# Kernel tuning notes

Hardware: AMD Instinct MI355X
Metric: run time of the kernel (lower is better)

The kernel has to match this reference:

```python
import jax, jax.numpy as jnp
import numpy as np

B, S_SRC, D, H, DH, FF, L, V, W, NG = 2, 4093, 768, 12, 64, 3072, 2, 50265, 256, 3
S = S_SRC + NG            # 4096, multiple of one-sided window W=256
NC = S // W               # 16 chunks
EPS = 1e-5
CLS_IDS = (50261, 50262, 50263)
NEG = -1e9


def setup_inputs() -> dict:
    key = jax.random.key(0)
    ks = jax.random.split(key, 16)
    std = 0.02
    inp = {
        "src": jax.random.randint(ks[0], (B, S_SRC), 0, 50260),
        "mask_src": jnp.ones((B, S_SRC), dtype=bool),
        "cluster_sizes": jax.random.randint(ks[1], (B,), 0, 16),
        "word_emb": jax.random.normal(ks[2], (V, D), jnp.float32) * std,
        "pos_emb": jax.random.normal(ks[3], (S, D), jnp.float32) * std,
        "emb_ln": jnp.stack([jnp.ones((D,)), jnp.zeros((D,))]),              # [2,D] scale,bias
        "attn_w": jax.random.normal(ks[4], (L, 7, D, D), jnp.float32) * std,  # q,k,v,qg,kg,vg,o
        "attn_b": jnp.zeros((L, 7, D), jnp.float32),
        "ln_p": jnp.stack([jnp.stack([jnp.ones((D,)), jnp.zeros((D,)), jnp.ones((D,)), jnp.zeros((D,))]) for _ in range(L)]),  # [L,4,D]
        "ffn_w1": jax.random.normal(ks[5], (L, D, FF), jnp.float32) * std,
        "ffn_b1": jnp.zeros((L, FF), jnp.float32),
        "ffn_w2": jax.random.normal(ks[6], (L, FF, D), jnp.float32) * std,
        "ffn_b2": jnp.zeros((L, D), jnp.float32),
        "cls_w": jax.random.normal(ks[7], (3, D), jnp.float32) * std,
        "cls_b": jnp.zeros((3,), jnp.float32),
    }
    return inp


def _ln(x, scale, bias):
    mu = jnp.mean(x, axis=-1, keepdims=True)
    var = jnp.mean(jnp.square(x - mu), axis=-1, keepdims=True)
    return (x - mu) * jax.lax.rsqrt(var + EPS) * scale + bias


def _encoder(ids, mask, word_emb, pos_emb, emb_ln, attn_w, attn_b, ln_p,
             ffn_w1, ffn_b1, ffn_w2, ffn_b2):
    x = _ln(word_emb[ids] + pos_emb[None, :S], emb_ln[0], emb_ln[1])  # [B,S,D]

    # static banded-attention index structure (chunk of W queries sees 3W keys)
    idx = np.arange(NC)[:, None] * W + np.arange(3 * W)[None, :]  # into padded seq
    kp = idx - W                                                   # absolute key pos
    valid = (kp >= 0) & (kp < S)
    kpc = jnp.asarray(np.clip(kp, 0, S - 1))
    qpos = np.arange(W)[:, None]
    band = jnp.asarray(np.abs(np.arange(3 * W)[None, :] - W - qpos) <= W)  # [W,3W]
    # global & padding keys removed from windowed attention (HF semantics)
    keymask = mask[:, kpc] & jnp.asarray(valid)[None] & jnp.asarray(kp >= NG)[None]  # [B,NC,3W]
    allowed = band[None, None] & keymask[:, :, None, :]  # [B,NC,W,3W]
    scale = 1.0 / np.sqrt(DH)

    def layer(x, p):
        aw, ab, lnp, w1, b1, w2, b2 = p
        def proj(i):
            return (x @ aw[i] + ab[i]).reshape(B, S, H, DH).transpose(0, 2, 1, 3)
        q = proj(0) * scale
        k = proj(1)
        v = proj(2)
        kpad = jnp.pad(k, ((0, 0), (0, 0), (W, W), (0, 0)))
        vpad = jnp.pad(v, ((0, 0), (0, 0), (W, W), (0, 0)))
        Kc = kpad[:, :, kpc + W]  # [B,H,NC,3W,DH] (kpc+W indexes padded)
        Vc = vpad[:, :, kpc + W]
        qc = q.reshape(B, H, NC, W, DH)
        s_loc = jnp.einsum('bhcqd,bhckd->bhcqk', qc, Kc)
        s_loc = jnp.where(allowed[:, None], s_loc, NEG)
        s_glb = jnp.einsum('bhcqd,bhgd->bhcqg', qc, k[:, :, :NG])  # all tokens -> global keys
        probs = jax.nn.softmax(jnp.concatenate([s_glb, s_loc], axis=-1), axis=-1)
        out = (jnp.einsum('bhcqg,bhgd->bhcqd', probs[..., :NG], v[:, :, :NG])
               + jnp.einsum('bhcqk,bhckd->bhcqd', probs[..., NG:], Vc))
        out = out.reshape(B, H, S, DH)
        # global query rows: full attention with global q/k/v projections
        qg = ((x[:, :NG] @ aw[3] + ab[3]).reshape(B, NG, H, DH)) * scale
        kg = (x @ aw[4] + ab[4]).reshape(B, S, H, DH)
        vg = (x @ aw[5] + ab[5]).reshape(B, S, H, DH)
        sg = jnp.einsum('bghd,bshd->bhgs', qg, kg)
        sg = jnp.where(mask[:, None, None, :], sg, NEG)
        og = jnp.einsum('bhgs,bshd->bhgd', jax.nn.softmax(sg, axis=-1), vg)
        out = out.at[:, :, :NG, :].set(og)
        out = out.transpose(0, 2, 1, 3).reshape(B, S, D)
        xa = _ln(x + out @ aw[6] + ab[6], lnp[0], lnp[1])
        h = jax.nn.gelu(xa @ w1 + b1, approximate=False)
        return _ln(xa + h @ w2 + b2, lnp[2], lnp[3]), None

    x, _ = jax.lax.scan(layer, x, (attn_w, attn_b, ln_p, ffn_w1, ffn_b1, ffn_w2, ffn_b2))
    return x


def reference(src, mask_src, cluster_sizes, word_emb, pos_emb, emb_ln, attn_w,
              attn_b, ln_p, ffn_w1, ffn_b1, ffn_w2, ffn_b2, cls_w, cls_b):
    ids = jnp.concatenate([jnp.broadcast_to(jnp.asarray(CLS_IDS), (B, NG)), src], axis=1)
    mask = jnp.concatenate([jnp.ones((B, NG), dtype=bool), mask_src], axis=1)
    h = _encoder(ids, mask, word_emb, pos_emb, emb_ln, attn_w, attn_b, ln_p,
                 ffn_w1, ffn_b1, ffn_w2, ffn_b2)  # [B,S,D]
    mf = mask.astype(h.dtype)
    scores = [jax.nn.sigmoid(h[:, i] @ cls_w[i] + cls_b[i]) * mf[:, i] for i in range(3)]
    verd, pros, cons = (s[:, None] for s in scores)
    return verd, pros, cons, mf[:, 0][:, None]
```

## Files before the change

### kernel.cpp

```cpp
#include <hip/hip_runtime.h>
#include <hip/hip_bf16.h>
#include <math.h>

#define B_    2
#define SSRC_ 4093
#define D_    768
#define H_    12
#define DH_   64
#define FF_   3072
#define NG_   3
#define W_    256
#define S_    4096
#define NC_   16
#define NSPLIT_ 16
#define QB_   128

typedef __attribute__((ext_vector_type(8))) short frag_ab;
typedef __attribute__((ext_vector_type(4))) float f32x4;

#define GL16(gp, lp) __builtin_amdgcn_global_load_lds( \
    (const __attribute__((address_space(1))) void*)(gp), \
    (__attribute__((address_space(3))) void*)(lp), 16, 0, 0)

__device__ __forceinline__ float bflo(unsigned int w) {
    union { float f; unsigned int i; } c; c.i = w << 16; return c.f;
}
__device__ __forceinline__ float bfhi(unsigned int w) {
    union { float f; unsigned int i; } c; c.i = w & 0xffff0000u; return c.f;
}
__device__ __forceinline__ void unp8(uint4 t, float* o) {
    o[0] = bflo(t.x); o[1] = bfhi(t.x); o[2] = bflo(t.y); o[3] = bfhi(t.y);
    o[4] = bflo(t.z); o[5] = bfhi(t.z); o[6] = bflo(t.w); o[7] = bfhi(t.w);
}
__device__ __forceinline__ unsigned short f2bfu(float x) {
    __hip_bfloat16 h = __float2bfloat16(x);
    return *reinterpret_cast<unsigned short*>(&h);
}

__device__ __forceinline__ float block_sum(float v, float* red) {
    int tid = threadIdx.x;
    red[tid] = v;
    __syncthreads();
#pragma unroll
    for (int off = 128; off >= 1; off >>= 1) {
        if (tid < off) red[tid] += red[tid + off];
        __syncthreads();
    }
    float r = red[0];
    __syncthreads();
    return r;
}

__device__ __forceinline__ float block_max(float v, float* red) {
    int tid = threadIdx.x;
    red[tid] = v;
    __syncthreads();
#pragma unroll
    for (int off = 128; off >= 1; off >>= 1) {
        if (tid < off) red[tid] = fmaxf(red[tid], red[tid + off]);
        __syncthreads();
    }
    float r = red[0];
    __syncthreads();
    return r;
}

__device__ __forceinline__ void storeO(float* p, float v) { *p = v; }
__device__ __forceinline__ void storeO(__hip_bfloat16* p, float v) { *p = __float2bfloat16(v); }

__global__ __launch_bounds__(256) void embed_ln_k(
    const int* __restrict__ src, const float* __restrict__ we,
    const float* __restrict__ pe, const float* __restrict__ gam,
    const float* __restrict__ bet, float* __restrict__ X,
    __hip_bfloat16* __restrict__ Xb) {
    __shared__ float red[256];
    int row = blockIdx.x;
    int b = row >> 12;
    int s = row & (S_ - 1);
    int tid = threadIdx.x;
    int id = (s < NG_) ? (50261 + s) : src[b * SSRC_ + (s - NG_)];
    const float* wr = we + (size_t)id * D_;
    const float* pr = pe + (size_t)s * D_;
    float v[3];
    float lsum = 0.f;
#pragma unroll
    for (int j = 0; j < 3; ++j) {
        int c = tid + j * 256;
        v[j] = wr[c] + pr[c];
        lsum += v[j];
    }
    float mu = block_sum(lsum, red) * (1.0f / 768.0f);
    float ls2 = 0.f;
#pragma unroll
    for (int j = 0; j < 3; ++j) { float d = v[j] - mu; ls2 += d * d; }
    float var = block_sum(ls2, red) * (1.0f / 768.0f);
    float rs = rsqrtf(var + 1e-5f);
    float* xr = X + (size_t)row * D_;
    __hip_bfloat16* xbr = Xb + (size_t)row * D_;
#pragma unroll
    for (int j = 0; j < 3; ++j) {
        int c = tid + j * 256;
        float o = (v[j] - mu) * rs * gam[c] + bet[c];
        xr[c] = o;
        xbr[c] = __float2bfloat16(o);
    }
}

__global__ __launch_bounds__(256) void residual_ln_k(
    const float* __restrict__ x, const float* __restrict__ y,
    const float* __restrict__ y2, const float* __restrict__ gam,
    const float* __restrict__ bet, float* __restrict__ out,
    __hip_bfloat16* __restrict__ outb) {
    __shared__ float red[256];
    int row = blockIdx.x;
    int tid = threadIdx.x;
    const float* xr = x + (size_t)row * D_;
    const float* yr = y + (size_t)row * D_;
    const float* y2r = y2 ? y2 + (size_t)row * D_ : nullptr;
    float v[3];
    float lsum = 0.f;
#pragma unroll
    for (int j = 0; j < 3; ++j) {
        int c = tid + j * 256;
        v[j] = xr[c] + yr[c];
        if (y2r) v[j] += y2r[c];
        lsum += v[j];
    }
    float mu = block_sum(lsum, red) * (1.0f / 768.0f);
    float ls2 = 0.f;
#pragma unroll
    for (int j = 0; j < 3; ++j) { float d = v[j] - mu; ls2 += d * d; }
    float var = block_sum(ls2, red) * (1.0f / 768.0f);
    float rs = rsqrtf(var + 1e-5f);
    float* orow = out + (size_t)row * D_;
    __hip_bfloat16* obr = outb ? outb + (size_t)row * D_ : nullptr;
#pragma unroll
    for (int j = 0; j < 3; ++j) {
        int c = tid + j * 256;
        float o = (v[j] - mu) * rs * gam[c] + bet[c];
        orow[c] = o;
        if (obr) obr[c] = __float2bfloat16(o);
    }
}

__global__ __launch_bounds__(256) void convt_k(
    const float* __restrict__ W, __hip_bfloat16* __restrict__ WT,
    int K, int N, int npb ) {
    __shared__ float tile[32][33];
    int mat = blockIdx.x / npb;
    int bx = blockIdx.x - mat * npb;
    int by = blockIdx.y;
    const float* Wm = W + (size_t)mat * K * N;
    __hip_bfloat16* WTm = WT + (size_t)mat * N * K;
    int tx = threadIdx.x & 31, ty = threadIdx.x >> 5;
#pragma unroll
    for (int i = 0; i < 32; i += 8)
        tile[ty + i][tx] = Wm[(size_t)(by * 32 + ty + i) * N + bx * 32 + tx];
    __syncthreads();
#pragma unroll
    for (int i = 0; i < 32; i += 8)
        WTm[(size_t)(bx * 32 + ty + i) * K + by * 32 + tx] = __float2bfloat16(tile[tx][ty + i]);
}

__global__ void pack_bias_k(const float* __restrict__ ab, float* __restrict__ dst) {
    int j = blockIdx.x * 256 + threadIdx.x;
    if (j >= 5 * 768) return;
    int mat = j / 768, c = j - mat * 768;
    int i = (mat < 3) ? mat : mat + 1;
    dst[j] = ab[i * 768 + c];
}

template <int EPI, int SPLIT>
__global__ __launch_bounds__(256) void mfma_gemm_k(
    const __hip_bfloat16* __restrict__ A, const __hip_bfloat16* __restrict__ BT,
    const float* __restrict__ bias, void* __restrict__ Cout,
    int M, int N, int K, size_t matstride) {
    __shared__ __align__(16) __hip_bfloat16 As[4096];
    __shared__ __align__(16) __hip_bfloat16 Bs[4096];
    int tid = threadIdx.x;
    int lane = tid & 63;
    int w = tid >> 6, wr = w >> 1, wc = w & 1;
    int brow = blockIdx.y * 128, bcol = blockIdx.x * 128;
    int z = blockIdx.z, nz = gridDim.z;
    int Kz = K / nz;
    int r0 = tid >> 2;
    int k0 = (((tid & 3) ^ (r0 & 3)) * 8);
    const __hip_bfloat16* Ag0 = A + (size_t)(brow + r0) * K + z * Kz + k0;
    const __hip_bfloat16* Ag1 = Ag0 + (size_t)64 * K;
    const __hip_bfloat16* Bg0 = BT + (size_t)(bcol + r0) * K + z * Kz + k0;
    const __hip_bfloat16* Bg1 = Bg0 + (size_t)64 * K;
    __hip_bfloat16* lA0 = &As[tid * 8];
    __hip_bfloat16* lA1 = &As[tid * 8 + 2048];
    __hip_bfloat16* lB0 = &Bs[tid * 8];
    __hip_bfloat16* lB1 = &Bs[tid * 8 + 2048];

    f32x4 acc[4][4];
#pragma unroll
    for (int m = 0; m < 4; ++m)
#pragma unroll
        for (int n = 0; n < 4; ++n) acc[m][n] = (f32x4){0.f, 0.f, 0.f, 0.f};

    int l15 = lane & 15, kb = lane >> 4;
    int xkb = kb ^ (l15 & 3);
    int aoff = (wr * 64 + l15) * 32 + xkb * 8;
    int boff = (wc * 64 + l15) * 32 + xkb * 8;

    for (int kt = 0; kt < Kz; kt += 32) {
        GL16(Ag0 + kt, lA0);
        GL16(Ag1 + kt, lA1);
        GL16(Bg0 + kt, lB0);
        GL16(Bg1 + kt, lB1);
        __syncthreads();
        frag_ab af[4], bf[4];
#pragma unroll
        for (int m = 0; m < 4; ++m) af[m] = *(const frag_ab*)&As[aoff + m * 512];
#pragma unroll
        for (int n = 0; n < 4; ++n) bf[n] = *(const frag_ab*)&Bs[boff + n * 512];
        __builtin_amdgcn_s_setprio(1);
#pragma unroll
        for (int m = 0; m < 4; ++m)
#pragma unroll
            for (int n = 0; n < 4; ++n)
                acc[m][n] = __builtin_amdgcn_mfma_f32_16x16x32_bf16(af[m], bf[n], acc[m][n], 0, 0, 0);
        __builtin_amdgcn_s_setprio(0);
        __syncthreads();
    }

    size_t zoff = (size_t)z * M * N;
#pragma unroll
    for (int m = 0; m < 4; ++m) {
        int rowb = brow + wr * 64 + m * 16 + (lane >> 4) * 4;
#pragma unroll
        for (int n = 0; n < 4; ++n) {
            int col = bcol + wc * 64 + n * 16 + l15;
            float bv = (z == 0) ? bias[col] : 0.f;
#pragma unroll
            for (int r = 0; r < 4; ++r) {
                float v = acc[m][n][r] + bv;
                size_t idx;
                if (SPLIT) {
                    int mat = col / 768;
                    idx = (size_t)mat * matstride + (size_t)(rowb + r) * 768 + (col - mat * 768);
                } else {
                    idx = zoff + (size_t)(rowb + r) * N + col;
                }
                if (EPI == 0) {
                    ((float*)Cout)[idx] = v;
                } else if (EPI == 1) {
                    ((__hip_bfloat16*)Cout)[idx] = __float2bfloat16(v);
                } else {
                    float g = 0.5f * v * (1.0f + erff(v * 0.70710678118654752f));
                    ((__hip_bfloat16*)Cout)[idx] = __float2bfloat16(g);
                }
            }
        }
    }
}

__global__ __launch_bounds__(256) void skinny_gemm_k(
    const float* __restrict__ A, const float* __restrict__ W,
    float* __restrict__ partial, int N, int K) {
    __shared__ float Asl[6][64];
    __shared__ float red[4][6][64];
    int tid = threadIdx.x;
    int cl = tid & 63;
    int kg = tid >> 6;
    int col = blockIdx.x * 64 + cl;
    int k0 = blockIdx.y * 64;
    for (int i = tid; i < 6 * 64; i += 256)
        Asl[i >> 6][i & 63] = A[(size_t)(i >> 6) * K + k0 + (i & 63)];
    __syncthreads();
    float acc[6] = {0.f, 0.f, 0.f, 0.f, 0.f, 0.f};
#pragma unroll
    for (int kk = 0; kk < 16; ++kk) {
        int k = kg * 16 + kk;
        float wv = W[(size_t)(k0 + k) * N + col];
#pragma unroll
        for (int m = 0; m < 6; ++m) acc[m] += Asl[m][k] * wv;
    }
#pragma unroll
    for (int m = 0; m < 6; ++m) red[kg][m][cl] = acc[m];
    __syncthreads();
    for (int i = tid; i < 6 * 64; i += 256) {
        int m = i >> 6, lane = i & 63;
        float s = red[0][m][lane] + red[1][m][lane] + red[2][m][lane] + red[3][m][lane];
        partial[(size_t)blockIdx.y * 6 * N + (size_t)m * N + blockIdx.x * 64 + lane] = s;
    }
}

__global__ __launch_bounds__(256) void skinny_reduce_k(
    const float* __restrict__ partial, const float* __restrict__ bias,
    float* __restrict__ outp, int N, int KS, int gelu) {
    int idx = blockIdx.x * 256 + threadIdx.x;
    if (idx >= 6 * N) return;
    int m = idx / N, col = idx - m * N;
    float s = bias[col];
    for (int kb = 0; kb < KS; ++kb)
        s += partial[(size_t)kb * 6 * N + (size_t)m * N + col];
    if (gelu) s = 0.5f * s * (1.0f + erff(s * 0.70710678118654752f));
    outp[(size_t)m * N + col] = s;
}

__global__ __launch_bounds__(256, 1) void local_attn_k(
    const __hip_bfloat16* __restrict__ Q, const __hip_bfloat16* __restrict__ K,
    const __hip_bfloat16* __restrict__ V, __hip_bfloat16* __restrict__ O) {
    __shared__ __align__(16) __hip_bfloat16 K_lds[64 * 72];
    __shared__ __align__(16) __hip_bfloat16 VT_lds[64 * 72];
    __shared__ __align__(16) __hip_bfloat16 P_lds[4][16 * 72];

    const int cq = blockIdx.x, h = blockIdx.y, b = blockIdx.z;
    const int tid = threadIdx.x;
    const int lane = tid & 63;
    const int w = tid >> 6;
    const int l15 = lane & 15, g4 = lane >> 4;
    const int cbase = cq * QB_;

    frag_ab qf[2][2];
#pragma unroll
    for (int qt = 0; qt < 2; ++qt) {
        int qa = cbase + w * 32 + qt * 16 + l15;
        const __hip_bfloat16* qp = Q + (size_t)(b * S_ + qa) * D_ + h * DH_ + g4 * 8;
        qf[qt][0] = *(const frag_ab*)qp;
        qf[qt][1] = *(const frag_ab*)(qp + 32);
    }

    f32x4 o[2][4];
#pragma unroll
    for (int qt = 0; qt < 2; ++qt)
#pragma unroll
        for (int dt = 0; dt < 4; ++dt) o[qt][dt] = (f32x4){0.f, 0.f, 0.f, 0.f};
    float mrun[2] = {-1e30f, -1e30f};
    float lrun[2] = {0.f, 0.f};

    int kw0 = cbase - W_; if (kw0 < 0) kw0 = 0;
    int kw1 = cbase + QB_ + W_; if (kw1 > S_) kw1 = S_;
    int ntiles = (kw1 - kw0) >> 6;

    char* Pw = (char*)P_lds[w];

    for (int t = 0; t < ntiles; ++t) {
        int k0 = kw0 + t * 64;
        __syncthreads();
        {
            const __hip_bfloat16* Kg = K + (size_t)(b * S_ + k0) * D_ + h * DH_;
            const __hip_bfloat16* Vg = V + (size_t)(b * S_ + k0) * D_ + h * DH_;
#pragma unroll
            for (int it = 0; it < 2; ++it) {
                int idx = tid + it * 256;
                int kk = idx >> 3, d0 = (idx & 7) * 8;
                uint4 kv = *(const uint4*)(Kg + (size_t)kk * D_ + d0);
                *(uint4*)&K_lds[kk * 72 + d0] = kv;
                uint4 vv = *(const uint4*)(Vg + (size_t)kk * D_ + d0);
                unsigned short vs[8];
                *(uint4*)vs = vv;
#pragma unroll
                for (int j = 0; j < 8; ++j) {
                    int dd = d0 + j;
                    int boff = dd * 144 + ((kk * 2) ^ (((dd >> 3) & 7) << 4));
                    *(unsigned short*)((char*)VT_lds + boff) = vs[j];
                }
            }
        }
        __syncthreads();

        frag_ab kf[4][2];
#pragma unroll
        for (int kt = 0; kt < 4; ++kt) {
            const char* kp = (const char*)K_lds + (kt * 16 + l15) * 144 + g4 * 16;
            kf[kt][0] = *(const frag_ab*)kp;
            kf[kt][1] = *(const frag_ab*)(kp + 64);
        }
        frag_ab vf[4][2];
#pragma unroll
        for (int dt = 0; dt < 4; ++dt) {
            int drow = dt * 16 + l15;
            int swz = ((drow >> 3) & 7) << 4;
            const char* vp = (const char*)VT_lds + drow * 144;
            vf[dt][0] = *(const frag_ab*)(vp + ((g4 * 16) ^ swz));
            vf[dt][1] = *(const frag_ab*)(vp + ((g4 * 16 + 64) ^ swz));
        }

#pragma unroll
        for (int qt = 0; qt < 2; ++qt) {
            f32x4 st[4];
            __builtin_amdgcn_s_setprio(1);
#pragma unroll
            for (int kt = 0; kt < 4; ++kt) {
                f32x4 z = (f32x4){0.f, 0.f, 0.f, 0.f};
                z = __builtin_amdgcn_mfma_f32_16x16x32_bf16(kf[kt][0], qf[qt][0], z, 0, 0, 0);
                z = __builtin_amdgcn_mfma_f32_16x16x32_bf16(kf[kt][1], qf[qt][1], z, 0, 0, 0);
                st[kt] = z;
            }
            __builtin_amdgcn_s_setprio(0);
            int qa = cbase + w * 32 + qt * 16 + l15;
            float sv[16];
            float mx = -1e30f;
#pragma unroll
            for (int kt = 0; kt < 4; ++kt)
#pragma unroll
                for (int r = 0; r < 4; ++r) {
                    int ka = k0 + kt * 16 + g4 * 4 + r;
                    float s = st[kt][r] * 0.125f;
                    bool bad = (ka < NG_) | (ka - qa > W_) | (qa - ka > W_);
                    s = bad ? -1e30f : s;
                    sv[kt * 4 + r] = s;
                    mx = fmaxf(mx, s);
                }
            mx = fmaxf(mx, __shfl_xor(mx, 16));
            mx = fmaxf(mx, __shfl_xor(mx, 32));
            float mnew = fmaxf(fmaxf(mrun[qt], mx), -60.0f);
            if (__any(mnew != mrun[qt])) {
                float fsc = __expf(mrun[qt] - mnew);
                mrun[qt] = mnew;
#pragma unroll
                for (int dt = 0; dt < 4; ++dt) o[qt][dt] *= fsc;
                lrun[qt] *= fsc;
            }
            float psum = 0.f;
            unsigned short pb[16];
#pragma unroll
            for (int i = 0; i < 16; ++i) {
                float p = __expf(sv[i] - mrun[qt]);
                psum += p;
                pb[i] = f2bfu(p);
            }
            psum += __shfl_xor(psum, 16);
            psum += __shfl_xor(psum, 32);
            lrun[qt] += psum;
#pragma unroll
            for (int kt = 0; kt < 4; ++kt)
#pragma unroll
                for (int rp = 0; rp < 2; ++rp) {
                    unsigned vpk = (unsigned)pb[kt * 4 + rp * 2] | ((unsigned)pb[kt * 4 + rp * 2 + 1] << 16);
                    int kloc = kt * 16 + g4 * 4 + rp * 2;
                    *(unsigned*)(Pw + l15 * 144 + kloc * 2) = vpk;
                }
            frag_ab pf0 = *(const frag_ab*)(Pw + l15 * 144 + g4 * 16);
            frag_ab pf1 = *(const frag_ab*)(Pw + l15 * 144 + g4 * 16 + 64);
            __builtin_amdgcn_s_setprio(1);
#pragma unroll
            for (int dt = 0; dt < 4; ++dt) {
                o[qt][dt] = __builtin_amdgcn_mfma_f32_16x16x32_bf16(vf[dt][0], pf0, o[qt][dt], 0, 0, 0);
                o[qt][dt] = __builtin_amdgcn_mfma_f32_16x16x32_bf16(vf[dt][1], pf1, o[qt][dt], 0, 0, 0);
            }
            __builtin_amdgcn_s_setprio(0);
        }
    }

    uint4 kgc[3][2];
    uint2 vgd[3][4];
#pragma unroll
    for (int gk = 0; gk < NG_; ++gk) {
        const __hip_bfloat16* kp = K + (size_t)(b * S_ + gk) * D_ + h * DH_ + g4 * 8;
        kgc[gk][0] = *(const uint4*)kp;
        kgc[gk][1] = *(const uint4*)(kp + 32);
        const __hip_bfloat16* vp = V + (size_t)(b * S_ + gk) * D_ + h * DH_ + g4 * 4;
#pragma unroll
        for (int dt = 0; dt < 4; ++dt)
            vgd[gk][dt] = *(const uint2*)(vp + dt * 16);
    }
#pragma unroll
    for (int qt = 0; qt < 2; ++qt) {
        float sg[3];
#pragma unroll
        for (int gk = 0; gk < NG_; ++gk) {
            float part = 0.f;
#pragma unroll
            for (int s = 0; s < 2; ++s) {
                uint4 qw = *(uint4*)&qf[qt][s];
                uint4 kw = kgc[gk][s];
                part += bflo(qw.x) * bflo(kw.x) + bfhi(qw.x) * bfhi(kw.x);
                part += bflo(qw.y) * bflo(kw.y) + bfhi(qw.y) * bfhi(kw.y);
                part += bflo(qw.z) * bflo(kw.z) + bfhi(qw.z) * bfhi(kw.z);
                part += bflo(qw.w) * bflo(kw.w) + bfhi(qw.w) * bfhi(kw.w);
            }
            part += __shfl_xor(part, 16);
            part += __shfl_xor(part, 32);
            sg[gk] = part * 0.125f;
        }
        float mx3 = fmaxf(fmaxf(sg[0], sg[1]), sg[2]);
        float mnew = fmaxf(fmaxf(mrun[qt], mx3), -60.0f);
        float fsc = __expf(mrun[qt] - mnew);
        mrun[qt] = mnew;
#pragma unroll
        for (int dt = 0; dt < 4; ++dt) o[qt][dt] *= fsc;
        lrun[qt] *= fsc;
        float pg[3];
        float psum = 0.f;
#pragma unroll
        for (int gk = 0; gk < NG_; ++gk) { pg[gk] = __expf(sg[gk] - mnew); psum += pg[gk]; }
        lrun[qt] += psum;
#pragma unroll
        for (int dt = 0; dt < 4; ++dt) {
#pragma unroll
            for (int gk = 0; gk < NG_; ++gk) {
                uint2 vv = vgd[gk][dt];
                o[qt][dt][0] += pg[gk] * bflo(vv.x);
                o[qt][dt][1] += pg[gk] * bfhi(vv.x);
                o[qt][dt][2] += pg[gk] * bflo(vv.y);
                o[qt][dt][3] += pg[gk] * bfhi(vv.y);
            }
        }
    }

#pragma unroll
    for (int qt = 0; qt < 2; ++qt) {
        float linv = 1.0f / lrun[qt];
        int qa = cbase + w * 32 + qt * 16 + l15;
        __hip_bfloat16* orow = O + (size_t)(b * S_ + qa) * D_ + h * DH_;
#pragma unroll
        for (int dt = 0; dt < 4; ++dt) {
            unsigned short pk[4];
#pragma unroll
            for (int r = 0; r < 4; ++r) pk[r] = f2bfu(o[qt][dt][r] * linv);
            *(uint2*)(orow + dt * 16 + g4 * 4) = *(uint2*)pk;
        }
    }
}

__global__ __launch_bounds__(256) void gattn_part_k(
    const float* __restrict__ qg, const __hip_bfloat16* __restrict__ KG,
    const __hip_bfloat16* __restrict__ VG, float* __restrict__ gpart) {
    __shared__ float sc[256];
    __shared__ float qs[DH_];
    __shared__ float red[256];
    __shared__ float rv[16][64];
    int split = blockIdx.x;
    int gh = blockIdx.y;
    int g = gh / H_, h = gh - g * H_;
    int b = blockIdx.z;
    int tid = threadIdx.x;
    if (tid < DH_) qs[tid] = qg[(size_t)(b * NG_ + g) * D_ + h * DH_ + tid] * 0.125f;
    __syncthreads();
    int s0 = split * (S_ / NSPLIT_);
    float acc = 0.f;
    {
        const __hip_bfloat16* kp = KG + (size_t)(b * S_ + s0 + tid) * D_ + h * DH_;
#pragma unroll
        for (int c8 = 0; c8 < 8; ++c8) {
            uint4 t = *(const uint4*)(kp + c8 * 8);
            float f[8]; unp8(t, f);
#pragma unroll
            for (int j = 0; j < 8; ++j) acc += qs[c8 * 8 + j] * f[j];
        }
    }
    float m = block_max(acc, red);
    float e = __expf(acc - m);
    sc[tid] = e;
    float l = block_sum(e, red);
    int sgq = tid >> 4, dq = (tid & 15) * 4;
    float a0 = 0.f, a1 = 0.f, a2 = 0.f, a3 = 0.f;
    const __hip_bfloat16* vbase = VG + (size_t)(b * S_ + s0 + sgq * 16) * D_ + h * DH_ + dq;
#pragma unroll
    for (int i = 0; i < 16; ++i) {
        float p = sc[sgq * 16 + i];
        uint2 vv = *(const uint2*)(vbase + (size_t)i * D_);
        a0 += p * bflo(vv.x); a1 += p * bfhi(vv.x);
        a2 += p * bflo(vv.y); a3 += p * bfhi(vv.y);
    }
    rv[sgq][dq] = a0; rv[sgq][dq + 1] = a1; rv[sgq][dq + 2] = a2; rv[sgq][dq + 3] = a3;
    __syncthreads();
    float* op = gpart + ((size_t)((b * NG_ + g) * H_ + h) * NSPLIT_ + split) * 66;
    if (tid == 0) { op[0] = m; op[1] = l; }
    if (tid < DH_) {
        float s = 0.f;
#pragma unroll
        for (int j = 0; j < 16; ++j) s += rv[j][tid];
        op[2 + tid] = s;
    }
}

template <typename TO>
__global__ __launch_bounds__(64) void gattn_comb_k(
    const float* __restrict__ gpart, TO* __restrict__ outp, int rowStride) {
    int g = blockIdx.x, h = blockIdx.y, b = blockIdx.z;
    int tid = threadIdx.x;
    const float* base = gpart + (size_t)((b * NG_ + g) * H_ + h) * NSPLIT_ * 66;
    float M = -1e30f;
#pragma unroll
    for (int p = 0; p < NSPLIT_; ++p) M = fmaxf(M, base[p * 66]);
    float l = 0.f, o = 0.f;
#pragma unroll
    for (int p = 0; p < NSPLIT_; ++p) {
        float wgt = __expf(base[p * 66] - M);
        l += wgt * base[p * 66 + 1];
        o += wgt * base[p * 66 + 2 + tid];
    }
    storeO(&outp[(size_t)(b * rowStride + g) * D_ + h * DH_ + tid], o / l);
}

__global__ void gather6_k(const float* __restrict__ X, float* __restrict__ xg) {
    int r = blockIdx.x;
    int b = r / NG_, g = r % NG_;
    for (int c = threadIdx.x; c < D_; c += blockDim.x)
        xg[(size_t)r * D_ + c] = X[(size_t)(b * S_ + g) * D_ + c];
}

__global__ __launch_bounds__(256) void classifier_k(
    const float* __restrict__ x26, const float* __restrict__ cw,
    const float* __restrict__ cb, float* __restrict__ out) {
    __shared__ float red[256];
    int tid = threadIdx.x;
    for (int i = 0; i < 3; ++i) {
        for (int b = 0; b < B_; ++b) {
            const float* xr = x26 + (size_t)(b * NG_ + i) * D_;
            const float* wr = cw + (size_t)i * D_;
            float p = 0.f;
            for (int c = tid; c < D_; c += 256) p += xr[c] * wr[c];
            float dotv = block_sum(p, red);
            if (tid == 0) out[i * B_ + b] = 1.0f / (1.0f + __expf(-(dotv + cb[i])));
        }
    }
    if (tid == 0) { out[6] = 1.0f; out[7] = 1.0f; }
}

extern "C" void kernel_launch(void* const* d_in, const int* in_sizes, int n_in,
                              void* d_out, int out_size, void* d_ws, size_t ws_size,
                              hipStream_t stream) {
    const int*   src      = (const int*)d_in[0];
    const float* word_emb = (const float*)d_in[3];
    const float* pos_emb  = (const float*)d_in[4];
    const float* emb_ln   = (const float*)d_in[5];
    const float* attn_w   = (const float*)d_in[6];
    const float* attn_b   = (const float*)d_in[7];
    const float* ln_p     = (const float*)d_in[8];
    const float* ffn_w1   = (const float*)d_in[9];
    const float* ffn_b1   = (const float*)d_in[10];
    const float* ffn_w2   = (const float*)d_in[11];
    const float* ffn_b2   = (const float*)d_in[12];
    const float* cls_w    = (const float*)d_in[13];
    const float* cls_b    = (const float*)d_in[14];
    float* out = (float*)d_out;

    const size_t NT = (size_t)B_ * S_ * D_;
    float* base = (float*)d_ws;
    float* X  = base;
    float* P4 = base + NT;
    __hip_bfloat16* Xb  = (__hip_bfloat16*)(base + 2 * NT);
    __hip_bfloat16* Qb  = (__hip_bfloat16*)(base + 5 * NT / 2);
    __hip_bfloat16* Kb  = (__hip_bfloat16*)(base + 3 * NT);
    __hip_bfloat16* Vb  = (__hip_bfloat16*)(base + 7 * NT / 2);
    __hip_bfloat16* KGb = (__hip_bfloat16*)(base + 4 * NT);
    __hip_bfloat16* VGb = (__hip_bfloat16*)(base + 9 * NT / 2);
    __hip_bfloat16* AOb = (__hip_bfloat16*)(base + 5 * NT);
    __hip_bfloat16* HCb = (__hip_bfloat16*)(base + 11 * NT / 2);
    float* pj1 = base + 15 * NT / 2;
    float* pj2 = base + 17 * NT / 2;
    __hip_bfloat16* wq5 = (__hip_bfloat16*)(base + 19 * NT / 2);
    __hip_bfloat16* wo  = wq5 + 5 * 589824;
    __hip_bfloat16* wg1 = wo + 589824;
    __hip_bfloat16* wf1 = wg1 + 2 * 589824;
    __hip_bfloat16* wf2 = wf1 + 2359296;
    float* SM  = (float*)(wf2 + 2359296);
    float* xg  = SM;
    float* qg6 = xg + 6 * D_;
    float* og6 = qg6 + 6 * D_;
    float* pr6 = og6 + 6 * D_;
    float* xa6 = pr6 + 6 * D_;
    float* h6  = xa6 + 6 * D_;
    float* f6  = h6 + 6 * FF_;
    float* x26 = f6 + 6 * D_;
    float* bias5 = x26 + 6 * D_;
    float* part = bias5 + 5 * D_;
    float* gpart = part;

    const int M = B_ * S_;
    dim3 blk(256);

    auto aw = [&](int l, int i) { return attn_w + ((size_t)(l * 7 + i)) * D_ * D_; };
    auto ab = [&](int l, int i) { return attn_b + (size_t)(l * 7 + i) * D_; };
    auto lnp = [&](int l, int i) { return ln_p + (size_t)(l * 4 + i) * D_; };

    auto skinny = [&](const float* A6, const float* Wm, const float* bias,
                      float* out6, int N, int K, int gelu) {
        skinny_gemm_k<<<dim3(N / 64, K / 64), blk, 0, stream>>>(A6, Wm, part, N, K);
        skinny_reduce_k<<<dim3((6 * N + 255) / 256), blk, 0, stream>>>(part, bias, out6, N, K / 64, gelu);
    };

    embed_ln_k<<<M, blk, 0, stream>>>(src, word_emb, pos_emb, emb_ln, emb_ln + D_, X, Xb);

    convt_k<<<dim3(24 * 3, 24), blk, 0, stream>>>(aw(0, 0), wq5, D_, D_, 24);
    convt_k<<<dim3(24 * 2, 24), blk, 0, stream>>>(aw(0, 4), wq5 + 3 * 589824, D_, D_, 24);
    pack_bias_k<<<15, blk, 0, stream>>>(ab(0, 0), bias5);
    mfma_gemm_k<1, 1><<<dim3(3840 / 128, 64), blk, 0, stream>>>(Xb, wq5, bias5, Qb, M, 3840, D_, NT);
    local_attn_k<<<dim3(S_ / QB_, H_, B_), blk, 0, stream>>>(Qb, Kb, Vb, AOb);
    gather6_k<<<B_ * NG_, blk, 0, stream>>>(X, xg);
    skinny(xg, aw(0, 3), ab(0, 3), qg6, D_, D_, 0);
    gattn_part_k<<<dim3(NSPLIT_, NG_ * H_, B_), blk, 0, stream>>>(qg6, KGb, VGb, gpart);
    gattn_comb_k<__hip_bfloat16><<<dim3(NG_, H_, B_), dim3(64), 0, stream>>>(gpart, AOb, S_);
    convt_k<<<dim3(24, 24), blk, 0, stream>>>(aw(0, 6), wo, D_, D_, 24);
    mfma_gemm_k<0, 0><<<dim3(6, 64, 2), blk, 0, stream>>>(AOb, wo, ab(0, 6), pj1, M, D_, D_, 0);
    residual_ln_k<<<M, blk, 0, stream>>>(X, pj1, pj2, lnp(0, 0), lnp(0, 1), P4, Xb);
    convt_k<<<dim3(96, 24), blk, 0, stream>>>(ffn_w1, wf1, D_, FF_, 96);
    convt_k<<<dim3(24, 96), blk, 0, stream>>>(ffn_w2, wf2, FF_, D_, 24);
    mfma_gemm_k<2, 0><<<dim3(24, 64), blk, 0, stream>>>(Xb, wf1, ffn_b1, HCb, M, FF_, D_, 0);
    mfma_gemm_k<0, 0><<<dim3(6, 64, 2), blk, 0, stream>>>(HCb, wf2, ffn_b2, pj1, M, D_, FF_, 0);
    residual_ln_k<<<M, blk, 0, stream>>>(P4, pj1, pj2, lnp(0, 2), lnp(0, 3), X, Xb);

    convt_k<<<dim3(24 * 2, 24), blk, 0, stream>>>(aw(1, 4), wg1, D_, D_, 24);
    mfma_gemm_k<1, 1><<<dim3(1536 / 128, 64), blk, 0, stream>>>(Xb, wg1, ab(1, 4), KGb, M, 1536, D_, NT);
    gather6_k<<<B_ * NG_, blk, 0, stream>>>(X, xg);
    skinny(xg, aw(1, 3), ab(1, 3), qg6, D_, D_, 0);
    gattn_part_k<<<dim3(NSPLIT_, NG_ * H_, B_), blk, 0, stream>>>(qg6, KGb, VGb, gpart);
    gattn_comb_k<float><<<dim3(NG_, H_, B_), dim3(64), 0, stream>>>(gpart, og6, NG_);
    skinny(og6, aw(1, 6), ab(1, 6), pr6, D_, D_, 0);
    residual_ln_k<<<B_ * NG_, blk, 0, stream>>>(xg, pr6, nullptr, lnp(1, 0), lnp(1, 1), xa6, nullptr);
    skinny(xa6, ffn_w1 + (size_t)D_ * FF_, ffn_b1 + FF_, h6, FF_, D_, 1);
    skinny(h6, ffn_w2 + (size_t)FF_ * D_, ffn_b2 + D_, f6, D_, FF_, 0);
    residual_ln_k<<<B_ * NG_, blk, 0, stream>>>(xa6, f6, nullptr, lnp(1, 2), lnp(1, 3), x26, nullptr);
    classifier_k<<<1, blk, 0, stream>>>(x26, cls_w, cls_b, out);
}
```

Baseline: 517.2 us.

## Triple-buffer GEMM LDS tiles with async prefetch and remap workgroup ids

The bf16 MFMA GEMM now keeps three LDS stages and issues global-to-LDS loads two k-tiles ahead. It waits on them with explicit vmcnt counts and a single barrier per tile, which is meant to hide global load latency behind MFMA work. It also remaps the workgroup linear id across groups of eight, likely to spread neighbouring tiles across XCDs for better L2 locality. The cost is triple the LDS footprint, which may reduce occupancy. The hand-written epilogue assumes the tile count nt is congruent to 0 mod 3 and at least 3; other K splits would compute incorrectly.

```diff
diff --git a/kernel.cpp b/kernel.cpp
--- a/kernel.cpp
+++ b/kernel.cpp
@@ -175,12 +175,19 @@
     const __hip_bfloat16* __restrict__ A, const __hip_bfloat16* __restrict__ BT,
     const float* __restrict__ bias, void* __restrict__ Cout,
     int M, int N, int K, size_t matstride) {
-    __shared__ __align__(16) __hip_bfloat16 As[4096];
-    __shared__ __align__(16) __hip_bfloat16 Bs[4096];
+    __shared__ __align__(16) __hip_bfloat16 As[3][4096];
+    __shared__ __align__(16) __hip_bfloat16 Bs[3][4096];
     int tid = threadIdx.x;
     int lane = tid & 63;
     int w = tid >> 6, wr = w >> 1, wc = w & 1;
-    int brow = blockIdx.y * 128, bcol = blockIdx.x * 128;
+    int nwg = gridDim.x * gridDim.y;
+    int id = blockIdx.y * gridDim.x + blockIdx.x;
+    if ((nwg & 7) == 0) {
+        int per = nwg >> 3;
+        id = (id & 7) * per + (id >> 3);
+    }
+    int bx = id % gridDim.x, by = id / gridDim.x;
+    int brow = by * 128, bcol = bx * 128;
     int z = blockIdx.z, nz = gridDim.z;
     int Kz = K / nz;
     int r0 = tid >> 2;
@@ -189,10 +196,6 @@
     const __hip_bfloat16* Ag1 = Ag0 + (size_t)64 * K;
     const __hip_bfloat16* Bg0 = BT + (size_t)(bcol + r0) * K + z * Kz + k0;
     const __hip_bfloat16* Bg1 = Bg0 + (size_t)64 * K;
-    __hip_bfloat16* lA0 = &As[tid * 8];
-    __hip_bfloat16* lA1 = &As[tid * 8 + 2048];
-    __hip_bfloat16* lB0 = &Bs[tid * 8];
-    __hip_bfloat16* lB1 = &Bs[tid * 8 + 2048];
 
     f32x4 acc[4][4];
 #pragma unroll
@@ -204,18 +207,21 @@
     int xkb = kb ^ (l15 & 3);
     int aoff = (wr * 64 + l15) * 32 + xkb * 8;
     int boff = (wc * 64 + l15) * 32 + xkb * 8;
-
-    for (int kt = 0; kt < Kz; kt += 32) {
-        GL16(Ag0 + kt, lA0);
-        GL16(Ag1 + kt, lA1);
-        GL16(Bg0 + kt, lB0);
-        GL16(Bg1 + kt, lB1);
-        __syncthreads();
+    int so = tid * 8;
+
+    auto stage = [&](int t, int bufi) {
+        int kt = t << 5;
+        GL16(Ag0 + kt, &As[bufi][so]);
+        GL16(Ag1 + kt, &As[bufi][so + 2048]);
+        GL16(Bg0 + kt, &Bs[bufi][so]);
+        GL16(Bg1 + kt, &Bs[bufi][so + 2048]);
+    };
+    auto compute = [&](int bufi) {
         frag_ab af[4], bf[4];
 #pragma unroll
-        for (int m = 0; m < 4; ++m) af[m] = *(const frag_ab*)&As[aoff + m * 512];
-#pragma unroll
-        for (int n = 0; n < 4; ++n) bf[n] = *(const frag_ab*)&Bs[boff + n * 512];
+        for (int m = 0; m < 4; ++m) af[m] = *(const frag_ab*)&As[bufi][aoff + m * 512];
+#pragma unroll
+        for (int n = 0; n < 4; ++n) bf[n] = *(const frag_ab*)&Bs[bufi][boff + n * 512];
         __builtin_amdgcn_s_setprio(1);
 #pragma unroll
         for (int m = 0; m < 4; ++m)
@@ -223,8 +229,31 @@
             for (int n = 0; n < 4; ++n)
                 acc[m][n] = __builtin_amdgcn_mfma_f32_16x16x32_bf16(af[m], bf[n], acc[m][n], 0, 0, 0);
         __builtin_amdgcn_s_setprio(0);
-        __syncthreads();
-    }
+    };
+
+    int nt = Kz >> 5;
+    stage(0, 0);
+    stage(1, 1);
+    asm volatile("s_waitcnt vmcnt(4)" ::: "memory");
+    asm volatile("s_barrier" ::: "memory");
+    for (int t = 0; t < nt - 3; t += 3) {
+        stage(t + 2, 2); compute(0);
+        asm volatile("s_waitcnt vmcnt(4)" ::: "memory");
+        asm volatile("s_barrier" ::: "memory");
+        stage(t + 3, 0); compute(1);
+        asm volatile("s_waitcnt vmcnt(4)" ::: "memory");
+        asm volatile("s_barrier" ::: "memory");
+        stage(t + 4, 1); compute(2);
+        asm volatile("s_waitcnt vmcnt(4)" ::: "memory");
+        asm volatile("s_barrier" ::: "memory");
+    }
+    stage(nt - 1, 2); compute(0);
+    asm volatile("s_waitcnt vmcnt(4)" ::: "memory");
+    asm volatile("s_barrier" ::: "memory");
+    compute(1);
+    asm volatile("s_waitcnt vmcnt(0)" ::: "memory");
+    asm volatile("s_barrier" ::: "memory");
+    compute(2);
 
     size_t zoff = (size_t)z * M * N;
 #pragma unroll
```

New measurement: 550.2 us. 6.4% more time.
